# Kernel tuning notes

Measured on AMD Instinct MI355X. Metric: run time of the kernel, lower is better.

The kernel has to match this reference:

```python
import jax, jax.numpy as jnp
import numpy as np
from jax import lax

B, H, W, C = 32, 64, 64, 192
DIN = 2 * C  # expand=2
EPS = 1e-5


def setup_inputs() -> dict:
    key = jax.random.key(0)
    ks = jax.random.split(key, 12)
    s = 0.02
    return {
        "x": jax.random.normal(ks[0], (B, H, W, C), dtype=jnp.float32),
        "norm_w": jnp.ones((C,), jnp.float32),
        "norm_b": jnp.zeros((C,), jnp.float32),
        "sel_w1": jax.random.normal(ks[1], (16, 4), jnp.float32) * 0.5,
        "sel_b1": jnp.zeros((16,), jnp.float32),
        "sel_w2": jax.random.normal(ks[2], (4, 16), jnp.float32) * 0.5,
        "sel_b2": jnp.zeros((4,), jnp.float32),
        "fc1_w": jax.random.normal(ks[3], (DIN, C), jnp.float32) * s,
        "fc1_b": jnp.zeros((DIN,), jnp.float32),
        "conv_w": jax.random.normal(ks[4], (DIN, 1, 3), jnp.float32) * 0.3,
        "conv_b": jnp.zeros((DIN,), jnp.float32),
        "fc2_w": jax.random.normal(ks[5], (C, DIN), jnp.float32) * s,
        "fc2_b": jnp.zeros((C,), jnp.float32),
    }


def _scan_dir(x, d):
    # x: [B,H,W,C] -> [B,L,C]; dirs = ['h','v','d','a'] (v and d are identical)
    b, h, w, c = x.shape
    if d == 0:  # 'h'
        return x.reshape(b, h * w, c)
    if d in (1, 2):  # 'v' / 'd': transpose then flatten
        return x.transpose(0, 2, 1, 3).reshape(b, w * h, c)
    # 'a': flip W, transpose, flatten
    return jnp.flip(x, axis=2).transpose(0, 2, 1, 3).reshape(b, w * h, c)


def _seq_block(s, fc1_w, fc1_b, conv_w, conv_b, fc2_w, fc2_b):
    # s: [B,L,C]
    h = jnp.einsum('blc,dc->bld', s, fc1_w) + fc1_b  # [B,L,DIN]
    hc = h.transpose(0, 2, 1)  # [B,DIN,L]
    hc = lax.conv_general_dilated(
        hc, conv_w, window_strides=(1,), padding=[(1, 1)],
        dimension_numbers=('NCH', 'OIH', 'NCH'),
        feature_group_count=conv_w.shape[0])
    hc = hc + conv_b[None, :, None]
    h = jax.nn.gelu(hc.transpose(0, 2, 1), approximate=False)
    return jnp.einsum('bld,cd->blc', h, fc2_w) + fc2_b


def reference(x, norm_w, norm_b, sel_w1, sel_b1, sel_w2, sel_b2,
              fc1_w, fc1_b, conv_w, conv_b, fc2_w, fc2_b):
    b, h, w, c = x.shape
    # LayerNorm over channels
    mu = x.mean(-1, keepdims=True)
    var = ((x - mu) ** 2).mean(-1, keepdims=True)
    xn = (x - mu) / jnp.sqrt(var + EPS) * norm_w + norm_b

    # Gradient-based direction selector
    g = xn.mean(-1)[:, None]  # [B,1,H,W]
    gp = jnp.pad(g, ((0, 0), (0, 0), (1, 1), (1, 1)), mode='reflect')
    grad_h = jnp.abs(gp[:, :, :, 2:] - gp[:, :, :, :-2])  # [B,1,H+2,W]
    grad_v = jnp.abs(gp[:, :, 2:, :] - gp[:, :, :-2, :])  # [B,1,H,W+2]
    sh = grad_h.mean(axis=(2, 3))  # [B,1]
    sv = grad_v.mean(axis=(2, 3))
    scores = jnp.concatenate([sh, sv, (sh + sv) / 2, jnp.abs(sh - sv)], axis=1)
    hid = jax.nn.relu(scores @ sel_w1.T + sel_b1)
    logits = hid @ sel_w2.T + sel_b2  # [B,4]
    dir_idx = jnp.argmax(logits, axis=-1)  # topk=1 -> argmax of softmax

    # Compute all 4 direction branches batched, then per-sample select
    outs = []
    for d in range(4):
        seq = _scan_dir(xn, d)
        proc = _seq_block(seq, fc1_w, fc1_b, conv_w, conv_b, fc2_w, fc2_b)
        outs.append(proc.reshape(b, h, w, c))  # unscan = plain reshape (as in source)
    stacked = jnp.stack(outs)  # [4,B,H,W,C]
    sel = stacked[dir_idx, jnp.arange(b)]  # [B,H,W,C]
    return x + sel
```

## Files before the change

kernel.cpp:

```cpp
#include <hip/hip_runtime.h>
#include <hip/hip_bf16.h>
#include <math.h>


typedef __bf16 bf16x8 __attribute__((ext_vector_type(8)));
typedef float f32x4 __attribute__((ext_vector_type(4)));
typedef __hip_bfloat16 hb;

#define XN_OFF   0
#define G_OFF    50331648
#define W1S_OFF  50855936
#define W2S_OFF  51003392
#define DIR_OFF  51150848

__device__ __forceinline__ float fast_gelu(float v) {
  float u = v * (0.7978845608f + 0.0356774081f * v * v);
  float e = __expf(2.f * u);
  float r = __builtin_amdgcn_rcpf(1.f + e);
  return v - v * r;
}

__device__ __forceinline__ unsigned short bf16bits(float f) {
  hb h = __float2bfloat16(f);
  return *reinterpret_cast<unsigned short*>(&h);
}

__global__ __launch_bounds__(256) void ln_wshuf_kernel(
    const float* __restrict__ x, const float* __restrict__ nw,
    const float* __restrict__ nb, hb* __restrict__ xn, float* __restrict__ g,
    const float* __restrict__ fc1_w, const float* __restrict__ fc2_w,
    hb* __restrict__ w1s, hb* __restrict__ w2s) {
  int t = threadIdx.x;
  if (blockIdx.x >= 8192) {
    int idx = (blockIdx.x - 8192) * 256 + t;
    const float* w; hb* o; int K, KS, li;
    if (idx < 73728) { w = fc1_w; o = w1s; K = 192; KS = 6;  li = idx; }
    else             { w = fc2_w; o = w2s; K = 384; KS = 12; li = idx - 73728; }
    int j = li & 7, lane = (li >> 3) & 63, f = li >> 9;
    int ks = f % KS, nt = f / KS;
    int n = nt * 16 + (lane & 15);
    int k = ks * 32 + ((lane >> 4) << 3) + j;
    o[li] = __float2bfloat16(w[n * K + k]);
    return;
  }
  __shared__ float4 xt[768];
  __shared__ unsigned int ytu[1536];
  __shared__ float snw[192], snb[192];
  long pixbase = (long)blockIdx.x * 16;
  const float4* x4 = (const float4*)(x + pixbase * 192);
  #pragma unroll
  for (int i = 0; i < 3; i++) xt[t + i * 256] = x4[t + i * 256];
  if (t < 192) { snw[t] = nw[t]; snb[t] = nb[t]; }
  __syncthreads();

  int p = t >> 4, sub = t & 15;
  const float4* row = xt + p * 48 + sub * 3;
  float4 f0 = row[0], f1 = row[1], f2 = row[2];
  float v[12] = {f0.x, f0.y, f0.z, f0.w, f1.x, f1.y, f1.z, f1.w,
                 f2.x, f2.y, f2.z, f2.w};
  float s1 = 0.f, s2 = 0.f;
  #pragma unroll
  for (int i = 0; i < 12; i++) { s1 += v[i]; s2 += v[i] * v[i]; }
  #pragma unroll
  for (int off = 8; off; off >>= 1) {
    s1 += __shfl_xor(s1, off);
    s2 += __shfl_xor(s2, off);
  }
  float mu = s1 * (1.f / 192.f);
  float var = s2 * (1.f / 192.f) - mu * mu;
  float rstd = rsqrtf(var + 1e-5f);
  int c0 = sub * 12;
  float ys[12], gs = 0.f;
  #pragma unroll
  for (int i = 0; i < 12; i++) {
    ys[i] = (v[i] - mu) * rstd * snw[c0 + i] + snb[c0 + i];
    gs += ys[i];
  }
  #pragma unroll
  for (int off = 8; off; off >>= 1) gs += __shfl_xor(gs, off);
  if (sub == 0) g[pixbase + p] = gs * (1.f / 192.f);
  unsigned int* yo = ytu + p * 96 + sub * 6;
  #pragma unroll
  for (int i = 0; i < 6; i++)
    yo[i] = (unsigned int)bf16bits(ys[2 * i]) |
            ((unsigned int)bf16bits(ys[2 * i + 1]) << 16);
  __syncthreads();
  const float4* yt4 = (const float4*)ytu;
  float4* o4 = (float4*)(xn + pixbase * 192);
  o4[t] = yt4[t];
  if (t < 128) o4[t + 256] = yt4[t + 256];
}

__global__ __launch_bounds__(256) void sel_kernel(
    const float* __restrict__ g, const float* __restrict__ w1,
    const float* __restrict__ b1, const float* __restrict__ w2,
    const float* __restrict__ b2, int* __restrict__ dir) {
  __shared__ float gt[64][65];
  __shared__ float red[8];
  int b = blockIdx.x, t = threadIdx.x;
  const float* gb = g + (long)b * 4096;
  for (int i = t; i < 4096; i += 256) gt[i >> 6][i & 63] = gb[i];
  __syncthreads();
  float ah = 0.f, av = 0.f;
  for (int i = t; i < 3968; i += 256) {
    int r = i / 62, j = i - r * 62 + 1;
    float d = fabsf(gt[r][j + 1] - gt[r][j - 1]);
    if (r == 1 || r == 62) d *= 2.f;
    ah += d;
  }
  for (int i = t; i < 3968; i += 256) {
    int r = (i >> 6) + 1, c = i & 63;
    float d = fabsf(gt[r + 1][c] - gt[r - 1][c]);
    if (c == 1 || c == 62) d *= 2.f;
    av += d;
  }
  #pragma unroll
  for (int off = 32; off; off >>= 1) {
    ah += __shfl_xor(ah, off);
    av += __shfl_xor(av, off);
  }
  if ((t & 63) == 0) { red[(t >> 6) * 2] = ah; red[(t >> 6) * 2 + 1] = av; }
  __syncthreads();
  if (t == 0) {
    float sh = 0.f, sv = 0.f;
    for (int w = 0; w < 4; w++) { sh += red[w * 2]; sv += red[w * 2 + 1]; }
    sh *= (1.f / 4224.f);
    sv *= (1.f / 4224.f);
    float sc[4] = {sh, sv, 0.5f * (sh + sv), fabsf(sh - sv)};
    float hid[16];
    #pragma unroll
    for (int i = 0; i < 16; i++) {
      float a = b1[i];
      for (int k = 0; k < 4; k++) a += sc[k] * w1[i * 4 + k];
      hid[i] = fmaxf(a, 0.f);
    }
    float best = -1e30f; int bi = 0;
    for (int j = 0; j < 4; j++) {
      float a = b2[j];
      for (int i = 0; i < 16; i++) a += hid[i] * w2[j * 16 + i];
      if (a > best) { best = a; bi = j; }
    }
    dir[b] = bi;
  }
}

#define SH_STR 196
__global__ __launch_bounds__(256, 4) void fused_kernel(
    const hb* __restrict__ xn, const hb* __restrict__ w1s, const hb* __restrict__ w2s,
    const float* __restrict__ fc1_b, const float* __restrict__ fc2_b,
    const float* __restrict__ conv_w, const float* __restrict__ conv_b,
    const float* __restrict__ x, const int* __restrict__ dirp,
    float* __restrict__ out) {
  __shared__ hb sH[2][32 * SH_STR];
  __shared__ float4 cvt[384];
  __shared__ float sB1[384];
  __shared__ float sB2[192];

  int b = blockIdx.y, mt = blockIdx.x;
  int dir = dirp[b];
  int l0 = mt * 30;
  int t = threadIdx.x;

  for (int d = t; d < 384; d += 256) {
    cvt[d] = make_float4(conv_w[d * 3], conv_w[d * 3 + 1], conv_w[d * 3 + 2], conv_b[d]);
    sB1[d] = fc1_b[d];
  }
  if (t < 192) sB2[t] = fc2_b[t];

  int wave = t >> 6, lane = t & 63;
  int m16 = lane & 15, q = lane >> 4;
  const hb* xnb = xn + (long)b * 4096 * 192;

  bf16x8 af[2][6];
  #pragma unroll
  for (int tl = 0; tl < 2; tl++) {
    int hr = tl * 16 + m16;
    int l = l0 - 1 + hr;
    int lc = min(max(l, 0), 4095);
    int src;
    if (dir == 0)      src = lc;
    else if (dir == 3) src = ((lc & 63) << 6) + 63 - (lc >> 6);
    else               src = ((lc & 63) << 6) + (lc >> 6);
    const bf16x8* ap = (const bf16x8*)(xnb + (long)src * 192) + q;
    #pragma unroll
    for (int ks = 0; ks < 6; ks++) af[tl][ks] = ap[ks * 4];
  }
  __syncthreads();

  {
    int buf = wave >> 1;
    int ntbase = wave * 6;
    #pragma unroll
    for (int i = 0; i < 6; i++) {
      int nt = ntbase + i;
      const bf16x8* bp = (const bf16x8*)w1s + (long)(nt * 6) * 64 + lane;
      f32x4 c0 = {0.f, 0.f, 0.f, 0.f}, c1 = {0.f, 0.f, 0.f, 0.f};
      #pragma unroll
      for (int ks = 0; ks < 6; ks++) {
        bf16x8 bf = bp[ks * 64];
        c0 = __builtin_amdgcn_mfma_f32_16x16x32_bf16(af[0][ks], bf, c0, 0, 0, 0);
        c1 = __builtin_amdgcn_mfma_f32_16x16x32_bf16(af[1][ks], bf, c1, 0, 0, 0);
      }
      float bias = sB1[nt * 16 + m16];
      int ncol = (nt - buf * 12) * 16 + m16;
      hb* s = &sH[buf][0];
      #pragma unroll
      for (int r = 0; r < 4; r++) {
        s[(q * 4 + r) * SH_STR + ncol]      = __float2bfloat16(c0[r] + bias);
        s[(16 + q * 4 + r) * SH_STR + ncol] = __float2bfloat16(c1[r] + bias);
      }
    }
  }
  __syncthreads();

  int tile2 = wave & 1, nth = wave >> 1;
  int hr = tile2 * 16 + m16;
  int l_c = l0 - 1 + hr;
  bool hm_ok = (l_c >= 1);
  bool hp_ok = (l_c <= 4094);
  int rm = hr > 0 ? hr - 1 : 0;
  int rp = hr < 31 ? hr + 1 : 31;
  bf16x8 z8 = {};
  const hb* base = &sH[nth][0];
  bf16x8 cg[6];
  #pragma unroll
  for (int i = 0; i < 6; i++) {
    int col = i * 32 + q * 8;
    bf16x8 vm = *(const bf16x8*)(base + rm * SH_STR + col);
    bf16x8 vc = *(const bf16x8*)(base + hr * SH_STR + col);
    bf16x8 vp = *(const bf16x8*)(base + rp * SH_STR + col);
    if (!hm_ok) vm = z8;
    if (!hp_ok) vp = z8;
    int d0 = (nth * 6 + i) * 32 + q * 8;
    bf16x8 o;
    #pragma unroll
    for (int j = 0; j < 8; j++) {
      float4 cw = cvt[d0 + j];
      float s = fmaf((float)vm[j], cw.x,
                fmaf((float)vc[j], cw.y,
                fmaf((float)vp[j], cw.z, cw.w)));
      o[j] = (__bf16)fast_gelu(s);
    }
    cg[i] = o;
  }
  __syncthreads();

  {
    hb* wb = &sH[nth][0];
    #pragma unroll
    for (int i = 0; i < 6; i++)
      *(bf16x8*)(wb + hr * SH_STR + i * 32 + q * 8) = cg[i];
  }

  f32x4 acc[6];
  #pragma unroll
  for (int i = 0; i < 6; i++) acc[i] = (f32x4){0.f, 0.f, 0.f, 0.f};
  const bf16x8* bp2 = (const bf16x8*)w2s + lane;
  #pragma unroll
  for (int i = 0; i < 6; i++) {
    int kk = nth * 6 + i;
    #pragma unroll
    for (int i2 = 0; i2 < 6; i2++) {
      int nt2 = nth * 6 + i2;
      acc[i2] = __builtin_amdgcn_mfma_f32_16x16x32_bf16(
          cg[i], bp2[((long)nt2 * 12 + kk) * 64], acc[i2], 0, 0, 0);
    }
  }
  __syncthreads();

  {
    const hb* ob = &sH[nth ^ 1][0];
    #pragma unroll
    for (int i = 0; i < 6; i++) {
      int kk = (nth ^ 1) * 6 + i;
      bf16x8 a = *(const bf16x8*)(ob + hr * SH_STR + i * 32 + q * 8);
      #pragma unroll
      for (int i2 = 0; i2 < 6; i2++) {
        int nt2 = nth * 6 + i2;
        acc[i2] = __builtin_amdgcn_mfma_f32_16x16x32_bf16(
            a, bp2[((long)nt2 * 12 + kk) * 64], acc[i2], 0, 0, 0);
      }
    }
  }

  #pragma unroll
  for (int i2 = 0; i2 < 6; i2++) {
    int c = (nth * 6 + i2) * 16 + m16;
    float bias = sB2[c];
    #pragma unroll
    for (int r = 0; r < 4; r++) {
      int hr_r = tile2 * 16 + q * 4 + r;
      int l_r = l0 - 1 + hr_r;
      if (hr_r >= 1 && hr_r <= 30 && l_r <= 4095) {
        long idx = ((long)b * 4096 + l_r) * 192 + c;
        out[idx] = x[idx] + acc[i2][r] + bias;
      }
    }
  }
}

extern "C" void kernel_launch(void* const* d_in, const int* in_sizes, int n_in,
                              void* d_out, int out_size, void* d_ws, size_t ws_size,
                              hipStream_t stream) {
  const float* x      = (const float*)d_in[0];
  const float* norm_w = (const float*)d_in[1];
  const float* norm_b = (const float*)d_in[2];
  const float* sel_w1 = (const float*)d_in[3];
  const float* sel_b1 = (const float*)d_in[4];
  const float* sel_w2 = (const float*)d_in[5];
  const float* sel_b2 = (const float*)d_in[6];
  const float* fc1_w  = (const float*)d_in[7];
  const float* fc1_b  = (const float*)d_in[8];
  const float* conv_w = (const float*)d_in[9];
  const float* conv_b = (const float*)d_in[10];
  const float* fc2_w  = (const float*)d_in[11];
  const float* fc2_b  = (const float*)d_in[12];
  float* out = (float*)d_out;
  char* ws = (char*)d_ws;

  hb* xn    = (hb*)(ws + XN_OFF);
  float* g  = (float*)(ws + G_OFF);
  hb* w1s   = (hb*)(ws + W1S_OFF);
  hb* w2s   = (hb*)(ws + W2S_OFF);
  int* dir  = (int*)(ws + DIR_OFF);

  ln_wshuf_kernel<<<8768, 256, 0, stream>>>(x, norm_w, norm_b, xn, g,
                                            fc1_w, fc2_w, w1s, w2s);
  sel_kernel<<<32, 256, 0, stream>>>(g, sel_w1, sel_b1, sel_w2, sel_b2, dir);
  dim3 gg(137, 32);
  fused_kernel<<<gg, 256, 0, stream>>>(xn, w1s, w2s, fc1_b, fc2_b,
                                       conv_w, conv_b, x, dir, out);
}
```

Baseline: 335.8 us.

## Split fused kernel work across 8 waves per block instead of 4

Doubles the fused kernel's block size to 512 threads and re-partitions each stage: fc1 N-tiles, conv+GELU column slices and fc2 output tiles are divided over 8 waves, each handling 3 tiles instead of 6. The goal is to cut per-wave serial MFMA and GELU work and per-thread register pressure, giving more latency hiding per block. The trade-off is that each wave now reads 9 of its 12 K-slices of the hidden activations from shared memory rather than 6. Launch bounds (512,4) may also cap registers per thread more tightly.

```diff
diff --git a/kernel.cpp b/kernel.cpp
--- a/kernel.cpp
+++ b/kernel.cpp
@@ -145,7 +145,7 @@
 }
 
 #define SH_STR 196
-__global__ __launch_bounds__(256, 4) void fused_kernel(
+__global__ __launch_bounds__(512, 4) void fused_kernel(
     const hb* __restrict__ xn, const hb* __restrict__ w1s, const hb* __restrict__ w2s,
     const float* __restrict__ fc1_b, const float* __restrict__ fc2_b,
     const float* __restrict__ conv_w, const float* __restrict__ conv_b,
@@ -161,9 +161,9 @@
   int l0 = mt * 30;
   int t = threadIdx.x;
 
-  for (int d = t; d < 384; d += 256) {
-    cvt[d] = make_float4(conv_w[d * 3], conv_w[d * 3 + 1], conv_w[d * 3 + 2], conv_b[d]);
-    sB1[d] = fc1_b[d];
+  if (t < 384) {
+    cvt[t] = make_float4(conv_w[t * 3], conv_w[t * 3 + 1], conv_w[t * 3 + 2], conv_b[t]);
+    sB1[t] = fc1_b[t];
   }
   if (t < 192) sB2[t] = fc2_b[t];
 
@@ -188,11 +188,10 @@
   __syncthreads();
 
   {
-    int buf = wave >> 1;
-    int ntbase = wave * 6;
-    #pragma unroll
-    for (int i = 0; i < 6; i++) {
-      int nt = ntbase + i;
+    int buf = wave >> 2;
+    #pragma unroll
+    for (int i = 0; i < 3; i++) {
+      int nt = wave * 3 + i;
       const bf16x8* bp = (const bf16x8*)w1s + (long)(nt * 6) * 64 + lane;
       f32x4 c0 = {0.f, 0.f, 0.f, 0.f}, c1 = {0.f, 0.f, 0.f, 0.f};
       #pragma unroll
@@ -213,7 +212,7 @@
   }
   __syncthreads();
 
-  int tile2 = wave & 1, nth = wave >> 1;
+  int tile2 = wave & 1, sq = wave >> 1;
   int hr = tile2 * 16 + m16;
   int l_c = l0 - 1 + hr;
   bool hm_ok = (l_c >= 1);
@@ -221,71 +220,71 @@
   int rm = hr > 0 ? hr - 1 : 0;
   int rp = hr < 31 ? hr + 1 : 31;
   bf16x8 z8 = {};
-  const hb* base = &sH[nth][0];
-  bf16x8 cg[6];
-  #pragma unroll
-  for (int i = 0; i < 6; i++) {
-    int col = i * 32 + q * 8;
+  bf16x8 cg[3];
+  #pragma unroll
+  for (int i = 0; i < 3; i++) {
+    int s = sq * 3 + i;
+    int bb = s >= 6 ? 1 : 0;
+    int col = (s - bb * 6) * 32 + q * 8;
+    const hb* base = &sH[bb][0];
     bf16x8 vm = *(const bf16x8*)(base + rm * SH_STR + col);
     bf16x8 vc = *(const bf16x8*)(base + hr * SH_STR + col);
     bf16x8 vp = *(const bf16x8*)(base + rp * SH_STR + col);
     if (!hm_ok) vm = z8;
     if (!hp_ok) vp = z8;
-    int d0 = (nth * 6 + i) * 32 + q * 8;
+    int d0 = s * 32 + q * 8;
     bf16x8 o;
     #pragma unroll
     for (int j = 0; j < 8; j++) {
       float4 cw = cvt[d0 + j];
-      float s = fmaf((float)vm[j], cw.x,
-                fmaf((float)vc[j], cw.y,
-                fmaf((float)vp[j], cw.z, cw.w)));
-      o[j] = (__bf16)fast_gelu(s);
+      float sv = fmaf((float)vm[j], cw.x,
+                 fmaf((float)vc[j], cw.y,
+                 fmaf((float)vp[j], cw.z, cw.w)));
+      o[j] = (__bf16)fast_gelu(sv);
     }
     cg[i] = o;
   }
   __syncthreads();
 
-  {
-    hb* wb = &sH[nth][0];
-    #pragma unroll
-    for (int i = 0; i < 6; i++)
-      *(bf16x8*)(wb + hr * SH_STR + i * 32 + q * 8) = cg[i];
-  }
-
-  f32x4 acc[6];
-  #pragma unroll
-  for (int i = 0; i < 6; i++) acc[i] = (f32x4){0.f, 0.f, 0.f, 0.f};
+  #pragma unroll
+  for (int i = 0; i < 3; i++) {
+    int s = sq * 3 + i;
+    int bb = s >= 6 ? 1 : 0;
+    *(bf16x8*)(&sH[bb][0] + hr * SH_STR + (s - bb * 6) * 32 + q * 8) = cg[i];
+  }
+
+  f32x4 acc[3];
+  #pragma unroll
+  for (int i = 0; i < 3; i++) acc[i] = (f32x4){0.f, 0.f, 0.f, 0.f};
   const bf16x8* bp2 = (const bf16x8*)w2s + lane;
   #pragma unroll
-  for (int i = 0; i < 6; i++) {
-    int kk = nth * 6 + i;
-    #pragma unroll
-    for (int i2 = 0; i2 < 6; i2++) {
-      int nt2 = nth * 6 + i2;
+  for (int i = 0; i < 3; i++) {
+    int kk = sq * 3 + i;
+    #pragma unroll
+    for (int i2 = 0; i2 < 3; i2++) {
+      int nt2 = sq * 3 + i2;
       acc[i2] = __builtin_amdgcn_mfma_f32_16x16x32_bf16(
           cg[i], bp2[((long)nt2 * 12 + kk) * 64], acc[i2], 0, 0, 0);
     }
   }
   __syncthreads();
 
-  {
-    const hb* ob = &sH[nth ^ 1][0];
-    #pragma unroll
-    for (int i = 0; i < 6; i++) {
-      int kk = (nth ^ 1) * 6 + i;
-      bf16x8 a = *(const bf16x8*)(ob + hr * SH_STR + i * 32 + q * 8);
-      #pragma unroll
-      for (int i2 = 0; i2 < 6; i2++) {
-        int nt2 = nth * 6 + i2;
-        acc[i2] = __builtin_amdgcn_mfma_f32_16x16x32_bf16(
-            a, bp2[((long)nt2 * 12 + kk) * 64], acc[i2], 0, 0, 0);
-      }
-    }
-  }
-
-  #pragma unroll
-  for (int i2 = 0; i2 < 6; i2++) {
-    int c = (nth * 6 + i2) * 16 + m16;
+  #pragma unroll
+  for (int j = 0; j < 9; j++) {
+    int kk = j < sq * 3 ? j : j + 3;
+    int bb = kk >= 6 ? 1 : 0;
+    bf16x8 a = *(const bf16x8*)(&sH[bb][0] + hr * SH_STR + (kk - bb * 6) * 32 + q * 8);
+    #pragma unroll
+    for (int i2 = 0; i2 < 3; i2++) {
+      int nt2 = sq * 3 + i2;
+      acc[i2] = __builtin_amdgcn_mfma_f32_16x16x32_bf16(
+          a, bp2[((long)nt2 * 12 + kk) * 64], acc[i2], 0, 0, 0);
+    }
+  }
+
+  #pragma unroll
+  for (int i2 = 0; i2 < 3; i2++) {
+    int c = (sq * 3 + i2) * 16 + m16;
     float bias = sB2[c];
     #pragma unroll
     for (int r = 0; r < 4; r++) {
@@ -328,6 +327,6 @@
                                             fc1_w, fc2_w, w1s, w2s);
   sel_kernel<<<32, 256, 0, stream>>>(g, sel_w1, sel_b1, sel_w2, sel_b2, dir);
   dim3 gg(137, 32);
-  fused_kernel<<<gg, 256, 0, stream>>>(xn, w1s, w2s, fc1_b, fc2_b,
+  fused_kernel<<<gg, 512, 0, stream>>>(xn, w1s, w2s, fc1_b, fc2_b,
                                        conv_w, conv_b, x, dir, out);
 }
```

New measurement: 372.6 us. 11.0% more time.
